# Optimization experiments

Hardware: AMD Instinct MI355X
Metric: run time of the kernel (lower is better)

## Reference

```python
import jax, jax.numpy as jnp
import numpy as np

N, T, D = 2, 4096, 1024
HD = 64          # head_dim
NH = D // HD     # 16 heads
W = 128          # sliding window size
BASE = 10000.0
EPS = 1.1920929e-07  # torch F.rms_norm default eps = float32 eps


def setup_inputs() -> dict:
    key = jax.random.key(0)
    k1, k2, k3, k4 = jax.random.split(key, 4)
    return {
        "input_NTD": jax.random.normal(k1, (N, T, D), jnp.float32),
        "qkv_weight": jax.random.normal(k2, (3, D, D), jnp.float32) / (D ** 0.5) / 2.0,
        "o_weight": jax.random.normal(k3, (D, D), jnp.float32) / (D ** 0.5) * 0.5,
        "o_scale": jax.random.normal(k4, (D,), jnp.float32) * 0.02,
    }


def _rms(x):
    x = x.astype(jnp.float32)
    return x * jax.lax.rsqrt(jnp.mean(x * x, axis=-1, keepdims=True) + EPS)


def reference(input_NTD, qkv_weight, o_weight, o_scale):
    # RMSNorm + fused QKV
    x = _rms(input_NTD)
    qkv = x @ qkv_weight.reshape(3 * D, D).T            # [N,T,3D]
    qkv = qkv.reshape(N, T, 3 * NH, HD)
    q, k, v = jnp.split(qkv, 3, axis=2)                 # each [N,T,NH,HD]
    q, k = _rms(q), _rms(k)
    # Rotary: freqs over head_dim//4 then zero-padded to head_dim//2
    nf = HD // 4
    freqs = (1.0 / BASE) ** jnp.linspace(0.0, 1.0, nf)
    freqs_d = jnp.concatenate([freqs, jnp.zeros_like(freqs)])       # [HD//2]
    theta = jnp.arange(T, dtype=jnp.float32)[:, None] * freqs_d     # [T,HD//2]
    cos = jnp.cos(theta)[None, :, None, :]
    sin = jnp.sin(theta)[None, :, None, :]
    def rot(z):
        z1, z2 = jnp.split(z, 2, axis=-1)
        return jnp.concatenate([z1 * cos + z2 * sin, -z1 * sin + z2 * cos], axis=-1)
    q, k = rot(q), rot(k)
    # [N,NH,T,HD] -> chunked sliding-window attention (chunk = W tokens)
    qh = q.transpose(0, 2, 1, 3)
    kh = k.transpose(0, 2, 1, 3)
    vh = v.transpose(0, 2, 1, 3).astype(jnp.float32)
    C = T // W
    qc = qh.reshape(N, NH, C, W, HD)
    kc = kh.reshape(N, NH, C, W, HD)
    vc = vh.reshape(N, NH, C, W, HD)
    kprev = jnp.concatenate([jnp.zeros_like(kc[:, :, :1]), kc[:, :, :-1]], axis=2)
    vprev = jnp.concatenate([jnp.zeros_like(vc[:, :, :1]), vc[:, :, :-1]], axis=2)
    kp = jnp.concatenate([kprev, kc], axis=3)           # [N,NH,C,2W,HD]
    vp = jnp.concatenate([vprev, vc], axis=3)
    scores = jnp.einsum('nhcqd,nhckd->nhcqk', qc, kp) / jnp.sqrt(jnp.float32(HD))
    j = jnp.arange(W)[:, None]
    m = jnp.arange(2 * W)[None, :]
    base = (m > j) & (m <= W + j)                       # 0 <= qpos-kpos < W
    chunk_ok = (jnp.arange(C)[:, None, None] > 0) | (m[None] >= W)
    mask = base[None] & chunk_ok                        # [C,W,2W]
    scores = jnp.where(mask[None, None], scores, -jnp.inf)
    probs = jax.nn.softmax(scores, axis=-1)
    out = jnp.einsum('nhcqk,nhckd->nhcqd', probs, vp)   # [N,NH,C,W,HD]
    out = out.reshape(N, NH, T, HD).transpose(0, 2, 1, 3).reshape(N, T, D)
    out = out.astype(input_NTD.dtype)
    # o_proj: FusedLinear with per-output scale, no bias
    o = out @ (o_weight * o_scale[:, None]).T
    return input_NTD + o
```

## Files before the change

### kernel.cpp

```cpp
#include <hip/hip_runtime.h>
#include <hip/hip_bf16.h>
#include <stdint.h>
#include <stddef.h>

#define T_S 4096
#define D_M 1024
#define NH_ 16
#define EPSF 1.1920929e-07f

typedef float f32x4 __attribute__((ext_vector_type(4)));
typedef __bf16 bf16x8 __attribute__((ext_vector_type(8)));
typedef short short8 __attribute__((ext_vector_type(8)));
typedef unsigned short ushort4v __attribute__((ext_vector_type(4)));

static __device__ __forceinline__ unsigned short f2bf(float f) {
  unsigned int u = __builtin_bit_cast(unsigned int, f);
  unsigned int r = (u + 0x7fffu + ((u >> 16) & 1u)) >> 16;
  return (unsigned short)r;
}

#define GLDS16(gp, lp) __builtin_amdgcn_global_load_lds( \
    (__attribute__((address_space(1))) void*)(gp),       \
    (__attribute__((address_space(3))) void*)(lp), 16, 0, 0)

static __device__ __forceinline__ f32x4 mfma16(bf16x8 a, bf16x8 b, f32x4 c) {
  return __builtin_amdgcn_mfma_f32_16x16x32_bf16(a, b, c, 0, 0, 0);
}

__global__ __launch_bounds__(256) void k_rope_tab(float* __restrict__ cosT,
                                                  float* __restrict__ sinT) {
  int i = blockIdx.x * 256 + threadIdx.x;
  int t = i >> 5, f = i & 31;
  float fr = (f < 16) ? powf(1e-4f, (float)f * (1.0f / 15.0f)) : 0.0f;
  float th = (float)t * fr;
  cosT[i] = cosf(th);
  sinT[i] = sinf(th);
}

__global__ __launch_bounds__(256) void k_f32_to_bf16(const float* __restrict__ src,
                                                     unsigned short* __restrict__ dst) {
  int i = blockIdx.x * 256 + threadIdx.x;
  float4 v = ((const float4*)src)[i];
  ushort4v o;
  o.x = f2bf(v.x); o.y = f2bf(v.y); o.z = f2bf(v.z); o.w = f2bf(v.w);
  ((ushort4v*)dst)[i] = o;
}

__global__ __launch_bounds__(256) void k_rmsnorm_cast(const float* __restrict__ x,
                                                      unsigned short* __restrict__ xn) {
  const int row = blockIdx.x;
  const int tid = threadIdx.x;
  float4 v = ((const float4*)(x + (size_t)row * D_M))[tid];
  float ss = v.x * v.x + v.y * v.y + v.z * v.z + v.w * v.w;
#pragma unroll
  for (int d = 1; d < 64; d <<= 1) ss += __shfl_xor(ss, d, 64);
  __shared__ float red[4];
  if ((tid & 63) == 0) red[tid >> 6] = ss;
  __syncthreads();
  float sc = rsqrtf((red[0] + red[1] + red[2] + red[3]) * (1.0f / D_M) + EPSF);
  ushort4v o;
  o.x = f2bf(v.x * sc); o.y = f2bf(v.y * sc); o.z = f2bf(v.z * sc); o.w = f2bf(v.w * sc);
  ((ushort4v*)(xn + (size_t)row * D_M))[tid] = o;
}

template <int EPI>
__global__ __launch_bounds__(512) void k_gemm256(
    const unsigned short* __restrict__ A, const unsigned short* __restrict__ B,
    unsigned short* __restrict__ q_out, unsigned short* __restrict__ k_out,
    unsigned short* __restrict__ v_out, float* __restrict__ Cf,
    const float* __restrict__ resid, const float* __restrict__ scale,
    const float* __restrict__ cosT, const float* __restrict__ sinT,
    int M, int Ncols, int K) {
  extern __shared__ __align__(16) char lds[];
  const int tid = threadIdx.x;
  const int lane = tid & 63, w = tid >> 6;
  const int lrow = lane & 15, g = lane >> 4;
  const int wm = w >> 1, wn = w & 1;
  const int m0 = blockIdx.y * 256, n0 = blockIdx.x * 128;
  const int NT = K >> 5;

  const int srcgrp = (((tid & 3) ^ ((tid >> 3) & 3)) << 3);
  const size_t aoff0 = (size_t)(m0 + (tid >> 2)) * K + srcgrp;
  const size_t aoff1 = aoff0 + (size_t)128 * K;
  const size_t boff = (size_t)(n0 + (tid >> 2)) * K + srcgrp;
  const int wbase = w * 1024;

  int abyte[4], bbyte[4];
#pragma unroll
  for (int i = 0; i < 4; ++i) {
    int ar = wm * 64 + i * 16 + lrow;
    abyte[i] = ar * 64 + ((g ^ ((ar >> 1) & 3)) << 4);
    int br = wn * 64 + i * 16 + lrow;
    bbyte[i] = 16384 + br * 64 + ((g ^ ((br >> 1) & 3)) << 4);
  }

  f32x4 acc[4][4] = {};

#pragma unroll
  for (int t = 0; t < 2; ++t) {
    char* sp = lds + t * 24576;
    GLDS16(A + aoff0 + t * 32, sp + wbase);
    GLDS16(A + aoff1 + t * 32, sp + 8192 + wbase);
    GLDS16(B + boff + t * 32, sp + 16384 + wbase);
  }
  asm volatile("s_waitcnt vmcnt(3)" ::: "memory");
  __builtin_amdgcn_s_barrier();
  asm volatile("" ::: "memory");

  int cb = 0, sb = 49152;
  for (int t = 0; t < NT; ++t) {
    if (t + 2 < NT) {
      const int kt2 = (t + 2) << 5;
      char* sp = lds + sb;
      GLDS16(A + aoff0 + kt2, sp + wbase);
      GLDS16(A + aoff1 + kt2, sp + 8192 + wbase);
      GLDS16(B + boff + kt2, sp + 16384 + wbase);
    }
    const char* cp = lds + cb;
    bf16x8 aF[4], bF[4];
#pragma unroll
    for (int i = 0; i < 4; ++i) aF[i] = *(const bf16x8*)(cp + abyte[i]);
#pragma unroll
    for (int i = 0; i < 4; ++i) bF[i] = *(const bf16x8*)(cp + bbyte[i]);
    __builtin_amdgcn_s_setprio(1);
#pragma unroll
    for (int mi = 0; mi < 4; ++mi)
#pragma unroll
      for (int ni = 0; ni < 4; ++ni)
        acc[mi][ni] = mfma16(aF[mi], bF[ni], acc[mi][ni]);
    __builtin_amdgcn_s_setprio(0);
    if (t + 2 < NT)
      asm volatile("s_waitcnt vmcnt(3)" ::: "memory");
    else
      asm volatile("s_waitcnt vmcnt(0)" ::: "memory");
    __builtin_amdgcn_s_barrier();
    asm volatile("" ::: "memory");
    cb += 24576; if (cb == 73728) cb = 0;
    sb += 24576; if (sb == 73728) sb = 0;
  }

  const int rbase = m0 + wm * 64 + g * 4;
  const int colbase = n0 + wn * 64;

  if (EPI == 1) {
#pragma unroll
    for (int mi = 0; mi < 4; ++mi)
#pragma unroll
      for (int nf = 0; nf < 4; ++nf) {
        int col = colbase + nf * 16 + lrow;
        float sc = scale[col];
#pragma unroll
        for (int j = 0; j < 4; ++j) {
          int row = rbase + mi * 16 + j;
          size_t idx = (size_t)row * Ncols + col;
          Cf[idx] = resid[idx] + sc * acc[mi][nf][j];
        }
      }
  } else {
    const int which = colbase >> 10;
    const int hh = (colbase >> 6) & 15;
    if (which == 2) {
#pragma unroll
      for (int mi = 0; mi < 4; ++mi)
#pragma unroll
        for (int j = 0; j < 4; ++j) {
          int row = rbase + mi * 16 + j;
          int t = row & (T_S - 1), nn = row >> 12;
          size_t ob = ((size_t)(nn * NH_ + hh) * T_S + t) * 64;
#pragma unroll
          for (int nf = 0; nf < 4; ++nf)
            v_out[ob + nf * 16 + lrow] = f2bf(acc[mi][nf][j]);
        }
    } else {
      unsigned short* dst = which ? k_out : q_out;
#pragma unroll
      for (int mi = 0; mi < 4; ++mi)
#pragma unroll
        for (int j = 0; j < 4; ++j) {
          int row = rbase + mi * 16 + j;
          int t = row & (T_S - 1), nn = row >> 12;
          float ss = 0.0f;
#pragma unroll
          for (int nf = 0; nf < 4; ++nf) ss += acc[mi][nf][j] * acc[mi][nf][j];
          ss += __shfl_xor(ss, 1, 64);
          ss += __shfl_xor(ss, 2, 64);
          ss += __shfl_xor(ss, 4, 64);
          ss += __shfl_xor(ss, 8, 64);
          float sc = rsqrtf(ss * (1.0f / 64.0f) + EPSF);
          size_t ob = ((size_t)(nn * NH_ + hh) * T_S + t) * 64;
#pragma unroll
          for (int nf = 0; nf < 2; ++nf) {
            int dd = nf * 16 + lrow;
            float cs = cosT[t * 32 + dd], sn = sinT[t * 32 + dd];
            float z1 = acc[mi][nf][j] * sc, z2 = acc[mi][nf + 2][j] * sc;
            dst[ob + dd] = f2bf(z1 * cs + z2 * sn);
            dst[ob + dd + 32] = f2bf(z2 * cs - z1 * sn);
          }
        }
    }
  }
}

__global__ __launch_bounds__(256) void k_attn(const unsigned short* __restrict__ qh,
                                              const unsigned short* __restrict__ kh,
                                              const unsigned short* __restrict__ vh,
                                              unsigned short* __restrict__ ao) {
  extern __shared__ __align__(16) char lds[];
  unsigned short* Vt = (unsigned short*)lds;
  unsigned short* Pb = (unsigned short*)(lds + 64 * 264 * 2);
  const int b = blockIdx.x;
  const int c = b & 31, nh = b >> 5;
  const int tid = threadIdx.x, lane = tid & 63, w = tid >> 6;
  const int lrow = lane & 15, g = lane >> 4, lk8 = g * 8;
  const size_t hb = (size_t)nh * T_S * 64;
  const unsigned short* qg = qh + hb + (size_t)c * 128 * 64;
  const unsigned short* kg = kh + hb + ((ptrdiff_t)c * 128 - 128) * 64;
  const unsigned short* vg = vh + hb + ((ptrdiff_t)c * 128 - 128) * 64;

  {
    const int m_idx = (tid & 7) | ((tid >> 6) << 3);
    const int m0v = m_idx * 8;
    const int d0 = ((tid >> 3) & 7) * 8;
    short8 vv[8];
#pragma unroll
    for (int i = 0; i < 8; ++i) {
      short8 z = {0, 0, 0, 0, 0, 0, 0, 0};
      if (!(c == 0 && m0v < 128)) z = *(const short8*)(vg + (size_t)(m0v + i) * 64 + d0);
      vv[i] = z;
    }
#pragma unroll
    for (int jj = 0; jj < 8; ++jj) {
      short8 wv;
#pragma unroll
      for (int i = 0; i < 8; ++i) wv[i] = vv[i][jj];
      *(short8*)(Vt + (size_t)(d0 + jj) * 264 + m0v) = wv;
    }
  }

  bf16x8 qf[2][2];
#pragma unroll
  for (int mi = 0; mi < 2; ++mi)
#pragma unroll
    for (int ks = 0; ks < 2; ++ks)
      qf[mi][ks] =
          *(const bf16x8*)(qg + (size_t)(w * 32 + mi * 16 + lrow) * 64 + ks * 32 + lk8);

  const int nlo = 2 * w;
  f32x4 s[2][10] = {};
#pragma unroll
  for (int u = 0; u < 10; ++u) {
    const int ni = nlo + u;
    if (c == 0 && ni < 8) continue;
    bf16x8 kf0 = *(const bf16x8*)(kg + (size_t)(ni * 16 + lrow) * 64 + lk8);
    bf16x8 kf1 = *(const bf16x8*)(kg + (size_t)(ni * 16 + lrow) * 64 + 32 + lk8);
#pragma unroll
    for (int mi = 0; mi < 2; ++mi) {
      s[mi][u] = mfma16(qf[mi][0], kf0, s[mi][u]);
      s[mi][u] = mfma16(qf[mi][1], kf1, s[mi][u]);
    }
  }

  float invs[2][4];
#pragma unroll
  for (int mi = 0; mi < 2; ++mi) {
#pragma unroll
    for (int j = 0; j < 4; ++j) {
      int jq = w * 32 + mi * 16 + g * 4 + j;
      float mx = -1e30f;
#pragma unroll
      for (int u = 0; u < 10; ++u) {
        int m = (nlo + u) * 16 + lrow;
        bool ok = (m > jq) && (m <= 128 + jq) && (c > 0 || m >= 128);
        float val = ok ? s[mi][u][j] * 0.125f : -1e30f;
        s[mi][u][j] = val;
        mx = fmaxf(mx, val);
      }
#pragma unroll
      for (int d2 = 1; d2 < 16; d2 <<= 1) mx = fmaxf(mx, __shfl_xor(mx, d2, 64));
      float sum = 0.0f;
#pragma unroll
      for (int u = 0; u < 10; ++u) {
        float p = __expf(s[mi][u][j] - mx);
        s[mi][u][j] = p;
        sum += p;
      }
#pragma unroll
      for (int d2 = 1; d2 < 16; d2 <<= 1) sum += __shfl_xor(sum, d2, 64);
      invs[mi][j] = 1.0f / sum;
    }
  }

  __syncthreads();

  f32x4 oacc[2][4] = {};
  unsigned short* Pw = Pb + w * (32 * 72);
  const int qlo = w >> 1;
#pragma unroll
  for (int qq = 0; qq < 3; ++qq) {
#pragma unroll
    for (int mi = 0; mi < 2; ++mi)
#pragma unroll
      for (int ni4 = 0; ni4 < 4; ++ni4)
#pragma unroll
        for (int j = 0; j < 4; ++j) {
          int r = mi * 16 + g * 4 + j;
          float val;
          if ((w & 1) == 0) {
            constexpr int base = 0;
            int u = qq * 4 + ni4 - base;
            val = (u >= 0 && u < 10) ? s[mi][(u >= 0 && u < 10) ? u : 0][j] : 0.0f;
          } else {
            int u = qq * 4 + ni4 - 2;
            val = (u >= 0 && u < 10) ? s[mi][(u >= 0 && u < 10) ? u : 0][j] : 0.0f;
          }
          Pw[r * 72 + ni4 * 16 + lrow] = f2bf(val);
        }
    const int qi = qlo + qq;
#pragma unroll
    for (int ks = 0; ks < 2; ++ks) {
      bf16x8 pf[2], vf[4];
#pragma unroll
      for (int mi = 0; mi < 2; ++mi)
        pf[mi] = *(const bf16x8*)&Pw[(mi * 16 + lrow) * 72 + ks * 32 + lk8];
#pragma unroll
      for (int nj = 0; nj < 4; ++nj)
        vf[nj] = *(const bf16x8*)&Vt[(nj * 16 + lrow) * 264 + qi * 64 + ks * 32 + lk8];
#pragma unroll
      for (int mi = 0; mi < 2; ++mi)
#pragma unroll
        for (int nj = 0; nj < 4; ++nj)
          oacc[mi][nj] = mfma16(pf[mi], vf[nj], oacc[mi][nj]);
    }
  }

  const int t0 = c * 128 + w * 32;
  const int n_ = nh >> 4, h_ = nh & 15;
#pragma unroll
  for (int mi = 0; mi < 2; ++mi)
#pragma unroll
    for (int nj = 0; nj < 4; ++nj)
#pragma unroll
      for (int j = 0; j < 4; ++j) {
        int t = t0 + mi * 16 + g * 4 + j;
        int dcol = nj * 16 + lrow;
        ao[((size_t)n_ * T_S + t) * D_M + h_ * 64 + dcol] =
            f2bf(oacc[mi][nj][j] * invs[mi][j]);
      }
}

extern "C" void kernel_launch(void* const* d_in, const int* in_sizes, int n_in,
                              void* d_out, int out_size, void* d_ws, size_t ws_size,
                              hipStream_t stream) {
  const float* x = (const float*)d_in[0];
  const float* qkvw = (const float*)d_in[1];
  const float* ow = (const float*)d_in[2];
  const float* osc = (const float*)d_in[3];
  float* out = (float*)d_out;

  char* ws = (char*)d_ws;
  unsigned short* xn = (unsigned short*)(ws + 0);
  unsigned short* qkvwb = (unsigned short*)(ws + 16777216);
  unsigned short* owb = (unsigned short*)(ws + 23068672);
  unsigned short* qhb = (unsigned short*)(ws + 25165824);
  unsigned short* khb = (unsigned short*)(ws + 41943040);
  unsigned short* vhb = (unsigned short*)(ws + 58720256);
  unsigned short* aob = (unsigned short*)(ws + 75497472);
  float* cosT = (float*)(ws + 92274688);
  float* sinT = (float*)(ws + 92798976);

  k_rope_tab<<<512, 256, 0, stream>>>(cosT, sinT);
  k_f32_to_bf16<<<3072, 256, 0, stream>>>(qkvw, qkvwb);
  k_f32_to_bf16<<<1024, 256, 0, stream>>>(ow, owb);
  k_rmsnorm_cast<<<8192, 256, 0, stream>>>(x, xn);
  k_gemm256<0><<<dim3(24, 32), 512, 73728, stream>>>(xn, qkvwb, qhb, khb, vhb, nullptr,
                                                     nullptr, nullptr, cosT, sinT,
                                                     8192, 3072, 1024);
  k_attn<<<1024, 256, 52224, stream>>>(qhb, khb, vhb, aob);
  k_gemm256<1><<<dim3(8, 32), 512, 73728, stream>>>(aob, owb, nullptr, nullptr, nullptr,
                                                    out, x, osc, nullptr, nullptr,
                                                    8192, 1024, 1024);
}
```

Baseline: 145.8 us.

## Restructure GEMM into 128x256 tiles with split-K-half double buffering and XCD remap

Replaces the 256x128 GEMM with a 128x256 tile that uses a 64-wide K step. The K step is split into two 32-wide halves across two LDS buffers, and each half's loads are issued while the other half's MFMAs run. Block IDs are remapped so neighbouring tiles land on the same XCD, which should improve L2 reuse. The LDS XOR swizzle is dropped, which risks bank conflicts on fragment reads. The larger 96KB LDS footprint may also limit how many blocks fit on a CU.

```diff
diff --git a/kernel.cpp b/kernel.cpp
--- a/kernel.cpp
+++ b/kernel.cpp
@@ -64,82 +64,100 @@
 }
 
 template <int EPI>
-__global__ __launch_bounds__(512) void k_gemm256(
+__global__ __launch_bounds__(512, 2) void k_gemm2p(
     const unsigned short* __restrict__ A, const unsigned short* __restrict__ B,
     unsigned short* __restrict__ q_out, unsigned short* __restrict__ k_out,
     unsigned short* __restrict__ v_out, float* __restrict__ Cf,
     const float* __restrict__ resid, const float* __restrict__ scale,
     const float* __restrict__ cosT, const float* __restrict__ sinT,
-    int M, int Ncols, int K) {
+    int cpx) {
   extern __shared__ __align__(16) char lds[];
   const int tid = threadIdx.x;
   const int lane = tid & 63, w = tid >> 6;
-  const int lrow = lane & 15, g = lane >> 4;
-  const int wm = w >> 1, wn = w & 1;
-  const int m0 = blockIdx.y * 256, n0 = blockIdx.x * 128;
-  const int NT = K >> 5;
-
-  const int srcgrp = (((tid & 3) ^ ((tid >> 3) & 3)) << 3);
-  const size_t aoff0 = (size_t)(m0 + (tid >> 2)) * K + srcgrp;
-  const size_t aoff1 = aoff0 + (size_t)128 * K;
-  const size_t boff = (size_t)(n0 + (tid >> 2)) * K + srcgrp;
-  const int wbase = w * 1024;
-
-  int abyte[4], bbyte[4];
-#pragma unroll
-  for (int i = 0; i < 4; ++i) {
-    int ar = wm * 64 + i * 16 + lrow;
-    abyte[i] = ar * 64 + ((g ^ ((ar >> 1) & 3)) << 4);
-    int br = wn * 64 + i * 16 + lrow;
-    bbyte[i] = 16384 + br * 64 + ((g ^ ((br >> 1) & 3)) << 4);
+  const int lrow = lane & 15, g4 = lane >> 4;
+  const int wm = w >> 2, wn = w & 3;
+  const int id = (blockIdx.x & 7) * cpx + (blockIdx.x >> 3);
+  const int m0 = (id & 63) * 128, n0 = (id >> 6) * 256;
+
+  auto stA = [&](int t, int kh, int dbx) {
+    const unsigned short* s =
+        A + (size_t)(m0 + (tid >> 2)) * 1024 + t * 64 + kh * 32 + ((tid & 3) << 3);
+    GLDS16(s, lds + dbx * 49152 + kh * 8192 + tid * 16);
+  };
+  auto stB = [&](int t, int kh, int dbx) {
+#pragma unroll
+    for (int it = 0; it < 2; ++it) {
+      int ci = it * 512 + tid;
+      const unsigned short* s =
+          B + (size_t)(n0 + (ci >> 2)) * 1024 + t * 64 + kh * 32 + ((ci & 3) << 3);
+      GLDS16(s, lds + dbx * 49152 + 16384 + kh * 16384 + ci * 16);
+    }
+  };
+
+  int a_off[2][4], b_off[2][4];
+#pragma unroll
+  for (int kh = 0; kh < 2; ++kh) {
+#pragma unroll
+    for (int i = 0; i < 4; ++i) {
+      a_off[kh][i] = kh * 8192 + (wm * 64 + i * 16 + lrow) * 64 + g4 * 16;
+      b_off[kh][i] = 16384 + kh * 16384 + (wn * 64 + i * 16 + lrow) * 64 + g4 * 16;
+    }
   }
 
   f32x4 acc[4][4] = {};
 
-#pragma unroll
-  for (int t = 0; t < 2; ++t) {
-    char* sp = lds + t * 24576;
-    GLDS16(A + aoff0 + t * 32, sp + wbase);
-    GLDS16(A + aoff1 + t * 32, sp + 8192 + wbase);
-    GLDS16(B + boff + t * 32, sp + 16384 + wbase);
-  }
+  stA(0, 0, 0); stB(0, 0, 0);
+  stA(0, 1, 0); stB(0, 1, 0);
+  stA(1, 0, 1); stB(1, 0, 1);
   asm volatile("s_waitcnt vmcnt(3)" ::: "memory");
   __builtin_amdgcn_s_barrier();
   asm volatile("" ::: "memory");
 
-  int cb = 0, sb = 49152;
-  for (int t = 0; t < NT; ++t) {
-    if (t + 2 < NT) {
-      const int kt2 = (t + 2) << 5;
-      char* sp = lds + sb;
-      GLDS16(A + aoff0 + kt2, sp + wbase);
-      GLDS16(A + aoff1 + kt2, sp + 8192 + wbase);
-      GLDS16(B + boff + kt2, sp + 16384 + wbase);
-    }
-    const char* cp = lds + cb;
-    bf16x8 aF[4], bF[4];
-#pragma unroll
-    for (int i = 0; i < 4; ++i) aF[i] = *(const bf16x8*)(cp + abyte[i]);
-#pragma unroll
-    for (int i = 0; i < 4; ++i) bF[i] = *(const bf16x8*)(cp + bbyte[i]);
-    __builtin_amdgcn_s_setprio(1);
-#pragma unroll
-    for (int mi = 0; mi < 4; ++mi)
-#pragma unroll
-      for (int ni = 0; ni < 4; ++ni)
-        acc[mi][ni] = mfma16(aF[mi], bF[ni], acc[mi][ni]);
-    __builtin_amdgcn_s_setprio(0);
-    if (t + 2 < NT)
-      asm volatile("s_waitcnt vmcnt(3)" ::: "memory");
-    else
-      asm volatile("s_waitcnt vmcnt(0)" ::: "memory");
-    __builtin_amdgcn_s_barrier();
-    asm volatile("" ::: "memory");
-    cb += 24576; if (cb == 73728) cb = 0;
-    sb += 24576; if (sb == 73728) sb = 0;
-  }
-
-  const int rbase = m0 + wm * 64 + g * 4;
+  for (int T = 0; T < 16; ++T) {
+    const int db = T & 1;
+    const char* cp = lds + db * 49152;
+    {
+      bf16x8 aF[4], bF[4];
+#pragma unroll
+      for (int i = 0; i < 4; ++i) aF[i] = *(const bf16x8*)(cp + a_off[0][i]);
+#pragma unroll
+      for (int i = 0; i < 4; ++i) bF[i] = *(const bf16x8*)(cp + b_off[0][i]);
+      if (T < 15) { stA(T + 1, 1, db ^ 1); stB(T + 1, 1, db ^ 1); }
+      __builtin_amdgcn_s_setprio(1);
+#pragma unroll
+      for (int mi = 0; mi < 4; ++mi)
+#pragma unroll
+        for (int ni = 0; ni < 4; ++ni)
+          acc[mi][ni] = mfma16(aF[mi], bF[ni], acc[mi][ni]);
+      __builtin_amdgcn_s_setprio(0);
+      asm volatile("" ::: "memory");
+      __builtin_amdgcn_s_barrier();
+      asm volatile("" ::: "memory");
+    }
+    {
+      bf16x8 aF[4], bF[4];
+#pragma unroll
+      for (int i = 0; i < 4; ++i) aF[i] = *(const bf16x8*)(cp + a_off[1][i]);
+#pragma unroll
+      for (int i = 0; i < 4; ++i) bF[i] = *(const bf16x8*)(cp + b_off[1][i]);
+      if (T < 14) { stA(T + 2, 0, db); stB(T + 2, 0, db); }
+      __builtin_amdgcn_s_setprio(1);
+#pragma unroll
+      for (int mi = 0; mi < 4; ++mi)
+#pragma unroll
+        for (int ni = 0; ni < 4; ++ni)
+          acc[mi][ni] = mfma16(aF[mi], bF[ni], acc[mi][ni]);
+      __builtin_amdgcn_s_setprio(0);
+      if (T < 14)
+        asm volatile("s_waitcnt vmcnt(3)" ::: "memory");
+      else
+        asm volatile("s_waitcnt vmcnt(0)" ::: "memory");
+      __builtin_amdgcn_s_barrier();
+      asm volatile("" ::: "memory");
+    }
+  }
+
+  const int rbase = m0 + wm * 64 + g4 * 4;
   const int colbase = n0 + wn * 64;
 
   if (EPI == 1) {
@@ -152,7 +170,7 @@
 #pragma unroll
         for (int j = 0; j < 4; ++j) {
           int row = rbase + mi * 16 + j;
-          size_t idx = (size_t)row * Ncols + col;
+          size_t idx = (size_t)row * 1024 + col;
           Cf[idx] = resid[idx] + sc * acc[mi][nf][j];
         }
       }
@@ -306,9 +324,8 @@
           int r = mi * 16 + g * 4 + j;
           float val;
           if ((w & 1) == 0) {
-            constexpr int base = 0;
-            int u = qq * 4 + ni4 - base;
-            val = (u >= 0 && u < 10) ? s[mi][(u >= 0 && u < 10) ? u : 0][j] : 0.0f;
+            int u = qq * 4 + ni4;
+            val = (u < 10) ? s[mi][u < 10 ? u : 0][j] : 0.0f;
           } else {
             int u = qq * 4 + ni4 - 2;
             val = (u >= 0 && u < 10) ? s[mi][(u >= 0 && u < 10) ? u : 0][j] : 0.0f;
@@ -372,11 +389,9 @@
   k_f32_to_bf16<<<3072, 256, 0, stream>>>(qkvw, qkvwb);
   k_f32_to_bf16<<<1024, 256, 0, stream>>>(ow, owb);
   k_rmsnorm_cast<<<8192, 256, 0, stream>>>(x, xn);
-  k_gemm256<0><<<dim3(24, 32), 512, 73728, stream>>>(xn, qkvwb, qhb, khb, vhb, nullptr,
-                                                     nullptr, nullptr, cosT, sinT,
-                                                     8192, 3072, 1024);
+  k_gemm2p<0><<<768, 512, 98304, stream>>>(xn, qkvwb, qhb, khb, vhb, nullptr,
+                                           nullptr, nullptr, cosT, sinT, 96);
   k_attn<<<1024, 256, 52224, stream>>>(qhb, khb, vhb, aob);
-  k_gemm256<1><<<dim3(8, 32), 512, 73728, stream>>>(aob, owb, nullptr, nullptr, nullptr,
-                                                    out, x, osc, nullptr, nullptr,
-                                                    8192, 1024, 1024);
-}
+  k_gemm2p<1><<<256, 512, 98304, stream>>>(aob, owb, nullptr, nullptr, nullptr, out,
+                                           x, osc, nullptr, nullptr, 32);
+}
```

Result: slower. 151.6 us (+4.0%).
